# Performance work log

Measured on AMD Instinct MI355X. Metric: run time of the kernel, lower is better.

## Reference

```python
import jax, jax.numpy as jnp
import numpy as np

N_ACTIVE = 32768
C = 512
B = 16
L = 4096


def setup_inputs() -> dict:
    key = jax.random.key(0)
    k1, k2 = jax.random.split(key)
    input_features = jax.random.normal(k1, (N_ACTIVE, C), dtype=jnp.float32)
    site_indices = jax.random.randint(k2, (N_ACTIVE,), 0, B * L, dtype=jnp.int64)
    return {
        "input_features": input_features,
        "site_indices": site_indices,
        "batch_size": B,
        "length": L,
    }


def reference(input_features, site_indices, batch_size, length):
    # Scatter each active-site feature row into its dense (batch, pos) slot.
    # Duplicate indices accumulate (matches SCN's summing behavior for
    # overlapping sites); untouched slots remain zero.
    c = input_features.shape[1]
    flat = jnp.zeros((batch_size * length, c), dtype=input_features.dtype)
    flat = flat.at[site_indices].add(input_features)
    return flat.reshape(batch_size, length, c)
```

## Files before the change

kernel.cpp:

```cpp
#include <hip/hip_runtime.h>


#define MAXD 12

typedef float f32x4 __attribute__((ext_vector_type(4)));

__global__ void fill_kernel(const int* __restrict__ idx, int* __restrict__ counts,
                            int* __restrict__ row_ids, int n) {
    int i = blockIdx.x * blockDim.x + threadIdx.x;
    if (i < n) {
        int d = idx[i];
        int pos = atomicAdd(&counts[d], 1);
        if (pos < MAXD) row_ids[d * MAXD + pos] = i;
    }
}

__global__ void __launch_bounds__(256) gather_kernel(
        const float* __restrict__ in,
        const int* __restrict__ counts,
        const int* __restrict__ row_ids,
        const int* __restrict__ idx,
        float* __restrict__ out, int C, int n_rows) {
    int wave = blockIdx.x * (blockDim.x >> 6) + (threadIdx.x >> 6);
    int lane = threadIdx.x & 63;

    int cnt  = counts[wave];
    int myid = (lane < MAXD) ? row_ids[wave * MAXD + lane] : -1;

    f32x4 a0 = 0.f;
    f32x4 a1 = 0.f;

    long col0 = (long)lane * 4;
    long col1 = (long)(C >> 1) + lane * 4;

    int m = (cnt < MAXD) ? cnt : MAXD;
    for (int j = 0; j < m; ++j) {
        int src = __shfl(myid, j);
        const f32x4* p0 = reinterpret_cast<const f32x4*>(in + (long)src * C + col0);
        const f32x4* p1 = reinterpret_cast<const f32x4*>(in + (long)src * C + col1);
        a0 += *p0;
        a1 += *p1;
    }

    if (cnt > MAXD) {
        for (int r = 0; r < n_rows; ++r) {
            if (__builtin_expect(idx[r] == wave, 0)) {
                bool captured = __any((lane < MAXD) && (myid == r));
                if (!captured) {
                    const f32x4* p0 = reinterpret_cast<const f32x4*>(in + (long)r * C + col0);
                    const f32x4* p1 = reinterpret_cast<const f32x4*>(in + (long)r * C + col1);
                    a0 += *p0;
                    a1 += *p1;
                }
            }
        }
    }

    *reinterpret_cast<f32x4*>(out + (long)wave * C + col0) = a0;
    *reinterpret_cast<f32x4*>(out + (long)wave * C + col1) = a1;
}

extern "C" void kernel_launch(void* const* d_in, const int* in_sizes, int n_in,
                              void* d_out, int out_size, void* d_ws, size_t ws_size,
                              hipStream_t stream) {
    const float* in  = (const float*)d_in[0];
    const int*   idx = (const int*)d_in[1];
    float*       out = (float*)d_out;

    int n_rows = in_sizes[1];
    int C      = in_sizes[0] / n_rows;
    int R      = out_size / C;

    int* counts  = (int*)d_ws;
    int* row_ids = counts + R;

    hipMemsetAsync(counts, 0, (size_t)R * sizeof(int), stream);

    int block = 256;
    fill_kernel<<<(n_rows + block - 1) / block, block, 0, stream>>>(idx, counts, row_ids, n_rows);

    int waves_per_block = block / 64;
    int grid = (R + waves_per_block - 1) / waves_per_block;
    gather_kernel<<<grid, block, 0, stream>>>(in, counts, row_ids, idx, out, C, n_rows);
}
```

Baseline: 41.22 us.

## Fuse bucketing and gather into one kernel with per-block shared-memory buckets

Replaces the memset, the global-atomic fill kernel and the gather kernel with a single kernel. Each block owns 32 output rows and scans the whole index array itself, bucketing matching source rows with shared-memory atomics before its four waves gather and sum feature rows. This removes two launches, the memset and the global counts/row_ids round trip. In exchange, every one of the ~2048 blocks re-reads the full index array, which adds a large amount of redundant L2 traffic and delays the start of each block's gather.

```diff
diff --git a/kernel.cpp b/kernel.cpp
--- a/kernel.cpp
+++ b/kernel.cpp
@@ -2,62 +2,89 @@
 
 
 #define MAXD 12
+#define RPB  32
 
 typedef float f32x4 __attribute__((ext_vector_type(4)));
+typedef int   i32x4 __attribute__((ext_vector_type(4)));
 
-__global__ void fill_kernel(const int* __restrict__ idx, int* __restrict__ counts,
-                            int* __restrict__ row_ids, int n) {
-    int i = blockIdx.x * blockDim.x + threadIdx.x;
-    if (i < n) {
-        int d = idx[i];
-        int pos = atomicAdd(&counts[d], 1);
-        if (pos < MAXD) row_ids[d * MAXD + pos] = i;
+__global__ void __launch_bounds__(256) fused_bucket_gather(
+        const float* __restrict__ in,
+        const int* __restrict__ idx,
+        float* __restrict__ out,
+        int C, int n_rows, int R) {
+    __shared__ int s_cnt[RPB];
+    __shared__ int s_ids[RPB][MAXD];
+
+    int base = blockIdx.x * RPB;
+
+    if (threadIdx.x < RPB) s_cnt[threadIdx.x] = 0;
+    __syncthreads();
+
+    int n4 = n_rows >> 2;
+    const i32x4* idx4 = reinterpret_cast<const i32x4*>(idx);
+    for (int i = threadIdx.x; i < n4; i += 256) {
+        i32x4 d4 = idx4[i];
+        int s0 = i << 2;
+        #pragma unroll
+        for (int k = 0; k < 4; ++k) {
+            unsigned rel = (unsigned)(d4[k] - base);
+            if (rel < (unsigned)RPB) {
+                int pos = atomicAdd(&s_cnt[rel], 1);
+                if (pos < MAXD) s_ids[rel][pos] = s0 + k;
+            }
+        }
     }
-}
+    for (int i = (n4 << 2) + threadIdx.x; i < n_rows; i += 256) {
+        unsigned rel = (unsigned)(idx[i] - base);
+        if (rel < (unsigned)RPB) {
+            int pos = atomicAdd(&s_cnt[rel], 1);
+            if (pos < MAXD) s_ids[rel][pos] = i;
+        }
+    }
+    __syncthreads();
 
-__global__ void __launch_bounds__(256) gather_kernel(
-        const float* __restrict__ in,
-        const int* __restrict__ counts,
-        const int* __restrict__ row_ids,
-        const int* __restrict__ idx,
-        float* __restrict__ out, int C, int n_rows) {
-    int wave = blockIdx.x * (blockDim.x >> 6) + (threadIdx.x >> 6);
+    int wid  = threadIdx.x >> 6;
     int lane = threadIdx.x & 63;
-
-    int cnt  = counts[wave];
-    int myid = (lane < MAXD) ? row_ids[wave * MAXD + lane] : -1;
-
-    f32x4 a0 = 0.f;
-    f32x4 a1 = 0.f;
 
     long col0 = (long)lane * 4;
     long col1 = (long)(C >> 1) + lane * 4;
 
-    int m = (cnt < MAXD) ? cnt : MAXD;
-    for (int j = 0; j < m; ++j) {
-        int src = __shfl(myid, j);
-        const f32x4* p0 = reinterpret_cast<const f32x4*>(in + (long)src * C + col0);
-        const f32x4* p1 = reinterpret_cast<const f32x4*>(in + (long)src * C + col1);
-        a0 += *p0;
-        a1 += *p1;
-    }
+    for (int r = wid; r < RPB; r += 4) {
+        int row = base + r;
+        if (row >= R) break;
 
-    if (cnt > MAXD) {
-        for (int r = 0; r < n_rows; ++r) {
-            if (__builtin_expect(idx[r] == wave, 0)) {
-                bool captured = __any((lane < MAXD) && (myid == r));
-                if (!captured) {
-                    const f32x4* p0 = reinterpret_cast<const f32x4*>(in + (long)r * C + col0);
-                    const f32x4* p1 = reinterpret_cast<const f32x4*>(in + (long)r * C + col1);
-                    a0 += *p0;
-                    a1 += *p1;
+        int cnt  = s_cnt[r];
+        int myid = (lane < MAXD) ? s_ids[r][lane] : -1;
+
+        f32x4 a0 = 0.f;
+        f32x4 a1 = 0.f;
+
+        int m = (cnt < MAXD) ? cnt : MAXD;
+        for (int j = 0; j < m; ++j) {
+            int src = __shfl(myid, j);
+            const f32x4* p0 = reinterpret_cast<const f32x4*>(in + (long)src * C + col0);
+            const f32x4* p1 = reinterpret_cast<const f32x4*>(in + (long)src * C + col1);
+            a0 += *p0;
+            a1 += *p1;
+        }
+
+        if (cnt > MAXD) {
+            for (int rr = 0; rr < n_rows; ++rr) {
+                if (__builtin_expect(idx[rr] == row, 0)) {
+                    bool captured = __any((lane < MAXD) && (myid == rr));
+                    if (!captured) {
+                        const f32x4* p0 = reinterpret_cast<const f32x4*>(in + (long)rr * C + col0);
+                        const f32x4* p1 = reinterpret_cast<const f32x4*>(in + (long)rr * C + col1);
+                        a0 += *p0;
+                        a1 += *p1;
+                    }
                 }
             }
         }
+
+        *reinterpret_cast<f32x4*>(out + (long)row * C + col0) = a0;
+        *reinterpret_cast<f32x4*>(out + (long)row * C + col1) = a1;
     }
-
-    *reinterpret_cast<f32x4*>(out + (long)wave * C + col0) = a0;
-    *reinterpret_cast<f32x4*>(out + (long)wave * C + col1) = a1;
 }
 
 extern "C" void kernel_launch(void* const* d_in, const int* in_sizes, int n_in,
@@ -71,15 +98,6 @@
     int C      = in_sizes[0] / n_rows;
     int R      = out_size / C;
 
-    int* counts  = (int*)d_ws;
-    int* row_ids = counts + R;
-
-    hipMemsetAsync(counts, 0, (size_t)R * sizeof(int), stream);
-
-    int block = 256;
-    fill_kernel<<<(n_rows + block - 1) / block, block, 0, stream>>>(idx, counts, row_ids, n_rows);
-
-    int waves_per_block = block / 64;
-    int grid = (R + waves_per_block - 1) / waves_per_block;
-    gather_kernel<<<grid, block, 0, stream>>>(in, counts, row_ids, idx, out, C, n_rows);
+    int grid = (R + RPB - 1) / RPB;
+    fused_bucket_gather<<<grid, 256, 0, stream>>>(in, idx, out, C, n_rows, R);
 }
```

New measurement: 44.55 us. +8.1%, slower.
